# Kernel tuning notes

Hardware: AMD Instinct MI355X
Metric: run time of the kernel (lower is better)

The kernel has to match this reference:

```python
import jax, jax.numpy as jnp
import numpy as np

D = 1024
HEADS = 16
HD = D // HEADS


def setup_inputs() -> dict:
    key = jax.random.key(0)
    kx, kqkv, kout = jax.random.split(key, 3)
    x = jax.random.normal(kx, (2, 2048, D), dtype=jnp.float32)
    # torch Linear weight is [out, in]; store same layout
    W_qkv = jax.random.normal(kqkv, (3 * D, D), dtype=jnp.float32) * (D ** -0.5)
    W_out = jax.random.normal(kout, (D, D), dtype=jnp.float32) * (D ** -0.5)
    return {"x": x, "W_qkv": W_qkv, "W_out": W_out}


def reference(x, W_qkv, W_out):
    B, T, _ = x.shape
    scale = HD ** -0.5
    qkv = jnp.einsum('btd,ed->bte', x, W_qkv)            # [B,T,3D]
    qkv = qkv.reshape(B, T, 3, HEADS, HD)
    q = jnp.transpose(qkv[:, :, 0], (0, 2, 1, 3))        # [B,H,T,hd]
    k = jnp.transpose(qkv[:, :, 1], (0, 2, 1, 3))
    v = jnp.transpose(qkv[:, :, 2], (0, 2, 1, 3))
    attn = jnp.einsum('bhqd,bhkd->bhqk', q, k) * scale   # [B,H,T,T]
    causal = jnp.tril(jnp.ones((T, T), dtype=bool))
    attn = jnp.where(causal, attn, -jnp.inf)
    attn = jax.nn.softmax(attn, axis=-1)
    out = jnp.einsum('bhqk,bhkd->bhqd', attn, v)         # [B,H,T,hd]
    out = jnp.transpose(out, (0, 2, 1, 3)).reshape(B, T, HEADS * HD)
    return jnp.einsum('btd,ed->bte', out, W_out)
```

## Files before the change

kernel.cpp:

```cpp
#include <hip/hip_runtime.h>
#include <cmath>


typedef unsigned short u16;
typedef unsigned int u32;
typedef short short8 __attribute__((ext_vector_type(8)));
typedef float floatx4 __attribute__((ext_vector_type(4)));

#define T_SZ 2048
#define HD_SZ 64
#define QSCALE 0.1803368801111244f

__device__ __forceinline__ u16 f2bf(float f) {
  unsigned u = __float_as_uint(f);
  u += 0x7fffu + ((u >> 16) & 1u);
  return (u16)(u >> 16);
}

__device__ __forceinline__ u32 pack_bf2(float lo, float hi) {
  return __builtin_amdgcn_perm(__float_as_uint(hi), __float_as_uint(lo), 0x07060302u);
}

__device__ __forceinline__ void gload16(const u16* g, u16* l) {
  __builtin_amdgcn_global_load_lds(
      (const __attribute__((address_space(1))) void*)g,
      (__attribute__((address_space(3))) void*)l, 16, 0, 0);
}

__global__ __launch_bounds__(256) void cast3(const float* __restrict__ a, u16* __restrict__ ao, int na4,
                                             const float* __restrict__ b, u16* __restrict__ bo, int nb4,
                                             const float* __restrict__ c, u16* __restrict__ co, int nc4) {
  int i = blockIdx.x * 256 + threadIdx.x;
  const float* src;
  u16* dst;
  int j;
  if (i < na4) { src = a; dst = ao; j = i; }
  else if (i < na4 + nb4) { src = b; dst = bo; j = i - na4; }
  else { j = i - na4 - nb4; if (j >= nc4) return; src = c; dst = co; }
  float4 f = ((const float4*)src)[j];
  ushort4 o;
  o.x = f2bf(f.x); o.y = f2bf(f.y); o.z = f2bf(f.z); o.w = f2bf(f.w);
  ((ushort4*)dst)[j] = o;
}

__global__ __launch_bounds__(256, 3) void gemm_qkv(const u16* __restrict__ A,
                                                   const u16* __restrict__ Bt,
                                                   u16* __restrict__ Qf,
                                                   u16* __restrict__ Kf,
                                                   u16* __restrict__ Vf) {
  __shared__ u16 SM[2 * 128 * 64];
  u16* As = SM;
  u16* Bs = SM + 128 * 64;
  const int Kdim = 1024;
  const int tid = threadIdx.x;
  const int lane = tid & 63;
  const int wave = tid >> 6;
  const int quad = lane >> 4;
  const int l16 = lane & 15;
  const int wm = wave >> 1, wn = wave & 1;
  const int m0 = blockIdx.y * 128;
  const int n0 = blockIdx.x * 128;

  floatx4 acc[4][4];
#pragma unroll
  for (int i = 0; i < 4; i++)
#pragma unroll
    for (int j = 0; j < 4; j++) acc[i][j] = (floatx4){0.f, 0.f, 0.f, 0.f};

  const int srow = lane >> 3;
  const int scol = ((lane & 7) ^ srow) * 8;
  const u16* gpA[4];
  const u16* gpB[4];
  u16 *lpA[4], *lpB[4];
#pragma unroll
  for (int u = 0; u < 4; u++) {
    const int row = wave * 32 + u * 8 + srow;
    gpA[u] = A + (size_t)(m0 + row) * Kdim + scol;
    gpB[u] = Bt + (size_t)(n0 + row) * Kdim + scol;
    lpA[u] = As + (wave * 32 + u * 8) * 64 + lane * 8;
    lpB[u] = Bs + (wave * 32 + u * 8) * 64 + lane * 8;
  }

  const int fsw = l16 & 7;

  for (int k0 = 0; k0 < Kdim; k0 += 64) {
    __syncthreads();
#pragma unroll
    for (int u = 0; u < 4; u++) {
      gload16(gpA[u] + k0, lpA[u]);
      gload16(gpB[u] + k0, lpB[u]);
    }
    __syncthreads();

#pragma unroll
    for (int h = 0; h < 2; h++) {
      const int seg = ((h * 4 + quad) ^ fsw) * 8;
      short8 af[4], bf[4];
#pragma unroll
      for (int mt = 0; mt < 4; mt++)
        af[mt] = *(const short8*)&As[(wm * 64 + mt * 16 + l16) * 64 + seg];
#pragma unroll
      for (int nt = 0; nt < 4; nt++)
        bf[nt] = *(const short8*)&Bs[(wn * 64 + nt * 16 + l16) * 64 + seg];
#pragma unroll
      for (int mt = 0; mt < 4; mt++)
#pragma unroll
        for (int nt = 0; nt < 4; nt++)
          acc[mt][nt] = __builtin_amdgcn_mfma_f32_16x16x32_bf16(af[mt], bf[nt], acc[mt][nt], 0, 0, 0);
    }
  }

  const int dest = n0 >> 10;
  const int n0w = n0 + wn * 64;
  const int m_abs = m0 + wm * 64;
  const int b = m_abs >> 11;
  const int t0w = m_abs & 2047;
  const int h = (n0w >> 6) & 15;
  const int bh = b * 16 + h;
  u16* dstp = (dest == 0) ? Qf : (dest == 1) ? Kf : Vf;

  auto do_epi = [&](u16* ep) {
    if (dest == 2) {
#pragma unroll
      for (int nt = 0; nt < 4; nt++) {
#pragma unroll
        for (int mt = 0; mt < 4; mt++) {
          uint2 w;
          w.x = (u32)f2bf(acc[mt][nt][0]) | ((u32)f2bf(acc[mt][nt][1]) << 16);
          w.y = (u32)f2bf(acc[mt][nt][2]) | ((u32)f2bf(acc[mt][nt][3]) << 16);
          *(uint2*)&ep[(nt * 16 + l16) * 72 + mt * 16 + quad * 4] = w;
        }
      }
    } else {
      const float sc = (dest == 0) ? QSCALE : 1.0f;
#pragma unroll
      for (int mt = 0; mt < 4; mt++)
#pragma unroll
        for (int nt = 0; nt < 4; nt++)
#pragma unroll
          for (int r = 0; r < 4; r++)
            ep[(mt * 16 + quad * 4 + r) * 72 + nt * 16 + l16] =
                f2bf(acc[mt][nt][r] * sc);
    }
#pragma unroll
    for (int blk = 0; blk < 8; blk++) {
      const int tgd = blk >> 1;
      const int half = blk & 1;
      const short8 v = *(const short8*)&ep[(tgd * 16 + l16) * 72 + half * 32 + quad * 8];
      size_t base;
      if (dest == 0)
        base = ((size_t)(bh * 128 + (t0w >> 4) + tgd) * 2 + half) * 512;
      else
        base = (((size_t)(bh * 32 + (t0w >> 6)) * 4 + tgd) * 2 + half) * 512;
      *(short8*)(dstp + base + lane * 8) = v;
    }
  };

  __syncthreads();
  if (wave < 2) do_epi(&SM[wave * 64 * 72]);
  __syncthreads();
  if (wave >= 2) do_epi(&SM[(wave - 2) * 64 * 72]);
}

__global__ __launch_bounds__(256, 4) void gemm_out(const u16* __restrict__ A,
                                                   const u16* __restrict__ Bt,
                                                   float* __restrict__ Cout) {
  __shared__ u16 As[64 * 64];
  __shared__ u16 Bs[128 * 64];
  const int Kdim = 1024;
  const int tid = threadIdx.x;
  const int lane = tid & 63;
  const int wave = tid >> 6;
  const int quad = lane >> 4;
  const int l16 = lane & 15;
  const int wm = wave >> 1, wn = wave & 1;
  const int m0 = blockIdx.y * 64;
  const int n0 = blockIdx.x * 128;

  floatx4 acc[2][4];
#pragma unroll
  for (int i = 0; i < 2; i++)
#pragma unroll
    for (int j = 0; j < 4; j++) acc[i][j] = (floatx4){0.f, 0.f, 0.f, 0.f};

  const int srow = lane >> 3;
  const int scol = ((lane & 7) ^ srow) * 8;
  const u16* gpA[2];
  const u16* gpB[4];
  u16 *lpA[2], *lpB[4];
#pragma unroll
  for (int u = 0; u < 2; u++) {
    const int row = wave * 16 + u * 8 + srow;
    gpA[u] = A + (size_t)(m0 + row) * Kdim + scol;
    lpA[u] = As + (wave * 16 + u * 8) * 64 + lane * 8;
  }
#pragma unroll
  for (int u = 0; u < 4; u++) {
    const int row = wave * 32 + u * 8 + srow;
    gpB[u] = Bt + (size_t)(n0 + row) * Kdim + scol;
    lpB[u] = Bs + (wave * 32 + u * 8) * 64 + lane * 8;
  }

  const int fsw = l16 & 7;

  for (int k0 = 0; k0 < Kdim; k0 += 64) {
    __syncthreads();
#pragma unroll
    for (int u = 0; u < 2; u++) gload16(gpA[u] + k0, lpA[u]);
#pragma unroll
    for (int u = 0; u < 4; u++) gload16(gpB[u] + k0, lpB[u]);
    __syncthreads();

#pragma unroll
    for (int h = 0; h < 2; h++) {
      const int seg = ((h * 4 + quad) ^ fsw) * 8;
      short8 af[2], bf[4];
#pragma unroll
      for (int mt = 0; mt < 2; mt++)
        af[mt] = *(const short8*)&As[(wm * 32 + mt * 16 + l16) * 64 + seg];
#pragma unroll
      for (int nt = 0; nt < 4; nt++)
        bf[nt] = *(const short8*)&Bs[(wn * 64 + nt * 16 + l16) * 64 + seg];
#pragma unroll
      for (int mt = 0; mt < 2; mt++)
#pragma unroll
        for (int nt = 0; nt < 4; nt++)
          acc[mt][nt] = __builtin_amdgcn_mfma_f32_16x16x32_bf16(af[mt], bf[nt], acc[mt][nt], 0, 0, 0);
    }
  }

#pragma unroll
  for (int mt = 0; mt < 2; mt++)
#pragma unroll
    for (int nt = 0; nt < 4; nt++)
#pragma unroll
      for (int r = 0; r < 4; r++) {
        const int m = m0 + wm * 32 + mt * 16 + quad * 4 + r;
        const int n = n0 + wn * 64 + nt * 16 + l16;
        Cout[(size_t)m * 1024 + n] = acc[mt][nt][r];
      }
}

__global__ __launch_bounds__(256, 2) void flash_attn(const u16* __restrict__ Qf,
                                                     const u16* __restrict__ Kf,
                                                     const u16* __restrict__ Vf,
                                                     u16* __restrict__ Og) {
  __shared__ u16 Ps[4][2][16 * 72];
  const int tid = threadIdx.x;
  const int lane = tid & 63, wave = tid >> 6;
  const int quad = lane >> 4, l16 = lane & 15;
  const int bh = blockIdx.x;
  const int py = blockIdx.y;
  const int p = (py < 8) ? py : 23 - py;
  const int gA = p, gB = 31 - p;
  const int b = bh >> 4, h = bh & 15;
  const u16* Qb = Qf + ((size_t)bh << 17);
  const u16* Kb = Kf + ((size_t)bh << 17);
  const u16* Vb = Vf + ((size_t)bh << 17);

  const u16* qpA = Qb + ((size_t)(gA * 4 + wave)) * 1024 + lane * 8;
  const u16* qpB = Qb + ((size_t)(gB * 4 + wave)) * 1024 + lane * 8;
  const short8 qfA0 = *(const short8*)qpA;
  const short8 qfA1 = *(const short8*)(qpA + 512);
  const short8 qfB0 = *(const short8*)qpB;
  const short8 qfB1 = *(const short8*)(qpB + 512);

  float lA = 0.f, lB = 0.f;
  floatx4 oA[4], oB[4];
#pragma unroll
  for (int dt = 0; dt < 4; dt++) {
    oA[dt] = (floatx4){0.f, 0.f, 0.f, 0.f};
    oB[dt] = (floatx4){0.f, 0.f, 0.f, 0.f};
  }
  u16* psA = &Ps[wave][0][0];
  u16* psB = &Ps[wave][1][0];

  short8 k0[4][2], v0[4][2];
  short8 k1[4][2], v1[4][2];

  auto load_tile = [&](int kt, short8 (*kk)[2], short8 (*vv)[2]) {
    const u16* kp = Kb + (size_t)kt * 4096 + lane * 8;
    const u16* vp = Vb + (size_t)kt * 4096 + lane * 8;
#pragma unroll
    for (int nt = 0; nt < 4; nt++) {
      kk[nt][0] = *(const short8*)(kp + (nt * 2 + 0) * 512);
      kk[nt][1] = *(const short8*)(kp + (nt * 2 + 1) * 512);
    }
#pragma unroll
    for (int dt = 0; dt < 4; dt++) {
      vv[dt][0] = *(const short8*)(vp + (dt * 2 + 0) * 512);
      vv[dt][1] = *(const short8*)(vp + (dt * 2 + 1) * 512);
    }
  };

  auto stream_step = [&](short8 (*ka)[2], short8 (*va)[2], bool diag,
                         const short8& qf0, const short8& qf1,
                         floatx4* o_acc, float& l_sum, u16* ps) {
    floatx4 sacc[4];
#pragma unroll
    for (int nt = 0; nt < 4; nt++) {
      if (diag && nt > wave) continue;
      floatx4 s = (floatx4){0.f, 0.f, 0.f, 0.f};
      s = __builtin_amdgcn_mfma_f32_16x16x32_bf16(ka[nt][0], qf0, s, 0, 0, 0);
      s = __builtin_amdgcn_mfma_f32_16x16x32_bf16(ka[nt][1], qf1, s, 0, 0, 0);
      sacc[nt] = s;
    }
#pragma unroll
    for (int nt = 0; nt < 4; nt++) {
      float p0 = 0.f, p1 = 0.f, p2 = 0.f, p3 = 0.f;
      if (!(diag && nt > wave)) {
        p0 = exp2f(sacc[nt][0]);
        p1 = exp2f(sacc[nt][1]);
        p2 = exp2f(sacc[nt][2]);
        p3 = exp2f(sacc[nt][3]);
        if (diag && nt == wave) {
          if (quad * 4 + 0 > l16) p0 = 0.f;
          if (quad * 4 + 1 > l16) p1 = 0.f;
          if (quad * 4 + 2 > l16) p2 = 0.f;
          if (quad * 4 + 3 > l16) p3 = 0.f;
        }
        l_sum += (p0 + p1) + (p2 + p3);
      }
      uint2 w;
      w.x = pack_bf2(p0, p1);
      w.y = pack_bf2(p2, p3);
      *(uint2*)&ps[l16 * 72 + nt * 16 + quad * 4] = w;
    }
    const short8 pf0 = *(const short8*)&ps[l16 * 72 + quad * 8];
    const short8 pf1 = *(const short8*)&ps[l16 * 72 + 32 + quad * 8];
    const bool skip_hi = diag && (wave < 2);
#pragma unroll
    for (int dt = 0; dt < 4; dt++) {
      o_acc[dt] = __builtin_amdgcn_mfma_f32_16x16x32_bf16(va[dt][0], pf0, o_acc[dt], 0, 0, 0);
      if (!skip_hi)
        o_acc[dt] = __builtin_amdgcn_mfma_f32_16x16x32_bf16(va[dt][1], pf1, o_acc[dt], 0, 0, 0);
    }
  };

  auto step_both = [&](int kt, short8 (*kk)[2], short8 (*vv)[2]) {
    stream_step(kk, vv, kt == gB, qfB0, qfB1, oB, lB, psB);
    if (kt <= gA) stream_step(kk, vv, kt == gA, qfA0, qfA1, oA, lA, psA);
  };

  load_tile(0, k0, v0);
  int kt = 0;
  for (;;) {
    if (kt < gB) load_tile(kt + 1, k1, v1);
    step_both(kt, k0, v0);
    if (++kt > gB) break;
    if (kt < gB) load_tile(kt + 1, k0, v0);
    step_both(kt, k1, v1);
    if (++kt > gB) break;
  }

  auto write_tile = [&](int g, floatx4* o_acc, float l_sum) {
    l_sum += __shfl_xor(l_sum, 16, 64);
    l_sum += __shfl_xor(l_sum, 32, 64);
    const float inv_l = 1.0f / l_sum;
    const int t0 = g * 64 + wave * 16;
    const size_t row = ((size_t)(b * 2048 + t0 + l16) << 10) + h * 64;
#pragma unroll
    for (int dt = 0; dt < 4; dt++) {
      uint2 w;
      w.x = pack_bf2(o_acc[dt][0] * inv_l, o_acc[dt][1] * inv_l);
      w.y = pack_bf2(o_acc[dt][2] * inv_l, o_acc[dt][3] * inv_l);
      *(uint2*)&Og[row + dt * 16 + quad * 4] = w;
    }
  };
  write_tile(gA, oA, lA);
  write_tile(gB, oB, lB);
}

extern "C" void kernel_launch(void* const* d_in, const int* in_sizes, int n_in,
                              void* d_out, int out_size, void* d_ws, size_t ws_size,
                              hipStream_t stream) {
  const float* x = (const float*)d_in[0];
  const float* Wqkv = (const float*)d_in[1];
  const float* Wout = (const float*)d_in[2];
  float* out = (float*)d_out;

  char* ws = (char*)d_ws;
  u16* xb    = (u16*)(ws + 0);
  u16* wqkvb = (u16*)(ws + 8388608);
  u16* woutb = (u16*)(ws + 14680064);
  u16* Qf    = (u16*)(ws + 16777216);
  u16* Kf    = (u16*)(ws + 25165824);
  u16* Vf    = (u16*)(ws + 33554432);
  u16* attn  = (u16*)(ws + 41943040);

  cast3<<<8192, 256, 0, stream>>>(x, xb, 1048576, Wqkv, wqkvb, 786432,
                                  Wout, woutb, 262144);

  gemm_qkv<<<dim3(24, 32), 256, 0, stream>>>(xb, wqkvb, Qf, Kf, Vf);

  flash_attn<<<dim3(32, 16), 256, 0, stream>>>(Qf, Kf, Vf, attn);

  gemm_out<<<dim3(8, 64), 256, 0, stream>>>(attn, woutb, out);
}
```

Before: 167.2 us.

## Share K/V tiles via LDS async loads and transpose P with permlane swaps

Each wave used to load the whole K/V tile from global into registers on its own. Now the four waves cooperatively load it once into a double-buffered LDS tile with global_load_lds, synchronised by __syncthreads, which cuts redundant global traffic fourfold. The P matrix no longer round-trips through per-wave LDS scratch: it is converted with v_cvt_pk_bf16_f32 and rearranged in registers with permlane32/16 swaps. In exchange, every tile step now needs a block-wide barrier and LDS reads of K/V, and the register P layout has to match what the MFMA expects.

```diff
diff --git a/kernel.cpp b/kernel.cpp
--- a/kernel.cpp
+++ b/kernel.cpp
@@ -19,6 +19,19 @@
 
 __device__ __forceinline__ u32 pack_bf2(float lo, float hi) {
   return __builtin_amdgcn_perm(__float_as_uint(hi), __float_as_uint(lo), 0x07060302u);
+}
+
+__device__ __forceinline__ u32 cvtpk(float a, float b) {
+  u32 r;
+  asm("v_cvt_pk_bf16_f32 %0, %1, %2" : "=v"(r) : "v"(a), "v"(b));
+  return r;
+}
+
+__device__ __forceinline__ void pl32swap(u32& a, u32& b) {
+  asm("v_permlane32_swap_b32 %0, %1" : "+v"(a), "+v"(b));
+}
+__device__ __forceinline__ void pl16swap(u32& a, u32& b) {
+  asm("v_permlane16_swap_b32 %0, %1" : "+v"(a), "+v"(b));
 }
 
 __device__ __forceinline__ void gload16(const u16* g, u16* l) {
@@ -245,7 +258,7 @@
                                                      const u16* __restrict__ Kf,
                                                      const u16* __restrict__ Vf,
                                                      u16* __restrict__ Og) {
-  __shared__ u16 Ps[4][2][16 * 72];
+  __shared__ __align__(16) u16 KV[2][16 * 512];
   const int tid = threadIdx.x;
   const int lane = tid & 63, wave = tid >> 6;
   const int quad = lane >> 4, l16 = lane & 15;
@@ -272,39 +285,36 @@
     oA[dt] = (floatx4){0.f, 0.f, 0.f, 0.f};
     oB[dt] = (floatx4){0.f, 0.f, 0.f, 0.f};
   }
-  u16* psA = &Ps[wave][0][0];
-  u16* psB = &Ps[wave][1][0];
-
-  short8 k0[4][2], v0[4][2];
-  short8 k1[4][2], v1[4][2];
-
-  auto load_tile = [&](int kt, short8 (*kk)[2], short8 (*vv)[2]) {
-    const u16* kp = Kb + (size_t)kt * 4096 + lane * 8;
-    const u16* vp = Vb + (size_t)kt * 4096 + lane * 8;
-#pragma unroll
-    for (int nt = 0; nt < 4; nt++) {
-      kk[nt][0] = *(const short8*)(kp + (nt * 2 + 0) * 512);
-      kk[nt][1] = *(const short8*)(kp + (nt * 2 + 1) * 512);
-    }
-#pragma unroll
-    for (int dt = 0; dt < 4; dt++) {
-      vv[dt][0] = *(const short8*)(vp + (dt * 2 + 0) * 512);
-      vv[dt][1] = *(const short8*)(vp + (dt * 2 + 1) * 512);
-    }
+
+  const u16* gkv[4];
+  u16* l0[4];
+  u16* l1[4];
+#pragma unroll
+  for (int i = 0; i < 4; i++) {
+    const int c = wave * 4 + i;
+    gkv[i] = ((c < 8) ? (Kb + c * 512) : (Vb + (c - 8) * 512)) + lane * 8;
+    l0[i] = &KV[0][c * 512] + lane * 8;
+    l1[i] = &KV[1][c * 512] + lane * 8;
+  }
+
+  auto load_tile = [&](int kt, u16* const* lp) {
+#pragma unroll
+    for (int i = 0; i < 4; i++) gload16(gkv[i] + (size_t)kt * 4096, lp[i]);
   };
 
-  auto stream_step = [&](short8 (*ka)[2], short8 (*va)[2], bool diag,
+  const floatx4 zero4 = {0.f, 0.f, 0.f, 0.f};
+
+  auto stream_step = [&](const short8 (*ka)[2], const short8 (*va)[2], bool diag,
                          const short8& qf0, const short8& qf1,
-                         floatx4* o_acc, float& l_sum, u16* ps) {
+                         floatx4* o_acc, float& l_sum) {
     floatx4 sacc[4];
 #pragma unroll
     for (int nt = 0; nt < 4; nt++) {
       if (diag && nt > wave) continue;
-      floatx4 s = (floatx4){0.f, 0.f, 0.f, 0.f};
-      s = __builtin_amdgcn_mfma_f32_16x16x32_bf16(ka[nt][0], qf0, s, 0, 0, 0);
-      s = __builtin_amdgcn_mfma_f32_16x16x32_bf16(ka[nt][1], qf1, s, 0, 0, 0);
-      sacc[nt] = s;
-    }
+      floatx4 s = __builtin_amdgcn_mfma_f32_16x16x32_bf16(ka[nt][0], qf0, zero4, 0, 0, 0);
+      sacc[nt] = __builtin_amdgcn_mfma_f32_16x16x32_bf16(ka[nt][1], qf1, s, 0, 0, 0);
+    }
+    u32 c[4][2];
 #pragma unroll
     for (int nt = 0; nt < 4; nt++) {
       float p0 = 0.f, p1 = 0.f, p2 = 0.f, p3 = 0.f;
@@ -321,13 +331,18 @@
         }
         l_sum += (p0 + p1) + (p2 + p3);
       }
-      uint2 w;
-      w.x = pack_bf2(p0, p1);
-      w.y = pack_bf2(p2, p3);
-      *(uint2*)&ps[l16 * 72 + nt * 16 + quad * 4] = w;
-    }
-    const short8 pf0 = *(const short8*)&ps[l16 * 72 + quad * 8];
-    const short8 pf1 = *(const short8*)&ps[l16 * 72 + 32 + quad * 8];
+      c[nt][0] = cvtpk(p0, p1);
+      c[nt][1] = cvtpk(p2, p3);
+    }
+    pl32swap(c[0][0], c[1][0]); pl16swap(c[0][0], c[1][0]);
+    pl32swap(c[0][1], c[1][1]); pl16swap(c[0][1], c[1][1]);
+    pl32swap(c[2][0], c[3][0]); pl16swap(c[2][0], c[3][0]);
+    pl32swap(c[2][1], c[3][1]); pl16swap(c[2][1], c[3][1]);
+    union { u32 w[4]; short8 s8; } P0, P1;
+    P0.w[0] = c[0][0]; P0.w[1] = c[0][1]; P0.w[2] = c[1][0]; P0.w[3] = c[1][1];
+    P1.w[0] = c[2][0]; P1.w[1] = c[2][1]; P1.w[2] = c[3][0]; P1.w[3] = c[3][1];
+    const short8 pf0 = P0.s8;
+    const short8 pf1 = P1.s8;
     const bool skip_hi = diag && (wave < 2);
 #pragma unroll
     for (int dt = 0; dt < 4; dt++) {
@@ -337,20 +352,34 @@
     }
   };
 
-  auto step_both = [&](int kt, short8 (*kk)[2], short8 (*vv)[2]) {
-    stream_step(kk, vv, kt == gB, qfB0, qfB1, oB, lB, psB);
-    if (kt <= gA) stream_step(kk, vv, kt == gA, qfA0, qfA1, oA, lA, psA);
+  auto compute = [&](int kt, const u16* Kl) {
+    short8 ka[4][2], va[4][2];
+#pragma unroll
+    for (int nt = 0; nt < 4; nt++)
+#pragma unroll
+      for (int hh = 0; hh < 2; hh++)
+        ka[nt][hh] = *(const short8*)&Kl[(nt * 2 + hh) * 512 + lane * 8];
+#pragma unroll
+    for (int dt = 0; dt < 4; dt++)
+#pragma unroll
+      for (int hh = 0; hh < 2; hh++)
+        va[dt][hh] = *(const short8*)&Kl[4096 + (dt * 2 + hh) * 512 + lane * 8];
+    stream_step(ka, va, kt == gB, qfB0, qfB1, oB, lB);
+    if (kt <= gA) stream_step(ka, va, kt == gA, qfA0, qfA1, oA, lA);
   };
 
-  load_tile(0, k0, v0);
+  load_tile(0, l0);
+  __syncthreads();
   int kt = 0;
   for (;;) {
-    if (kt < gB) load_tile(kt + 1, k1, v1);
-    step_both(kt, k0, v0);
+    if (kt < gB) load_tile(kt + 1, l1);
+    compute(kt, &KV[0][0]);
     if (++kt > gB) break;
-    if (kt < gB) load_tile(kt + 1, k0, v0);
-    step_both(kt, k1, v1);
+    __syncthreads();
+    if (kt < gB) load_tile(kt + 1, l0);
+    compute(kt, &KV[1][0]);
     if (++kt > gB) break;
+    __syncthreads();
   }
 
   auto write_tile = [&](int g, floatx4* o_acc, float l_sum) {
```

Result: faster. 160.2 us (-4.2%).
